# Optimization experiments

Measured on AMD Instinct MI355X. Metric: run time of the kernel, lower is better.

Reference implementation:

```python
import jax, jax.numpy as jnp
import numpy as np

T, B, OBS, LS, H, NA = 256, 1024, 128, 128, 128, 18


def setup_inputs() -> dict:
    key = jax.random.key(0)
    ks = jax.random.split(key, 20)
    rn = lambda i, shape, sc: jax.random.normal(ks[i], shape, dtype=jnp.float32) * sc
    return {
        "x": jax.random.normal(ks[0], (T * B, OBS), dtype=jnp.float32),
        "done": (jax.random.uniform(ks[1], (T * B,)) < 0.05).astype(jnp.float32),
        "h0": rn(2, (1, B, H), 0.1),
        "c0": rn(3, (1, B, H), 0.1),
        # MLP encoder: obs -> 128 -> 32 -> lstm_size
        "W1": rn(4, (128, OBS), 0.1), "b1": jnp.zeros((128,), jnp.float32),
        "W2": rn(5, (32, 128), 0.1), "b2": jnp.zeros((32,), jnp.float32),
        "W3": rn(6, (LS, 32), 0.1), "b3": jnp.zeros((LS,), jnp.float32),
        # LSTM params, PyTorch gate order [i, f, g, o]
        "Wih": rn(7, (4 * H, LS), 0.1), "Whh": rn(8, (4 * H, H), 0.1),
        "bih": jnp.zeros((4 * H,), jnp.float32), "bhh": jnp.zeros((4 * H,), jnp.float32),
        "Wa": rn(9, (NA, H), 0.01), "ba": jnp.zeros((NA,), jnp.float32),
        "Wc": rn(10, (1, H), 0.1), "bc": jnp.zeros((1,), jnp.float32),
    }


def reference(x, done, h0, c0, W1, b1, W2, b2, W3, b3, Wih, Whh, bih, bhh, Wa, ba, Wc, bc):
    # MLP encoder (self.network)
    hid = jax.nn.relu(x @ W1.T + b1)
    hid = jax.nn.relu(hid @ W2.T + b2)
    hid = jax.nn.relu(hid @ W3.T + b3)           # [T*B, LS]
    Bsz = h0.shape[1]
    hid = hid.reshape(-1, Bsz, hid.shape[-1])    # [T, B, LS]
    d = done.reshape(-1, Bsz)                    # [T, B]

    Hh = h0.shape[-1]

    def step(carry, inp):
        h, c = carry
        xt, dt = inp
        m = (1.0 - dt)[:, None]                  # reset mask
        h = h * m
        c = c * m
        gates = xt @ Wih.T + bih + h @ Whh.T + bhh   # [B, 4H]
        i = jax.nn.sigmoid(gates[:, :Hh])
        f = jax.nn.sigmoid(gates[:, Hh:2 * Hh])
        g = jnp.tanh(gates[:, 2 * Hh:3 * Hh])
        o = jax.nn.sigmoid(gates[:, 3 * Hh:])
        c = f * c + i * g
        h = o * jnp.tanh(c)
        return (h, c), h

    (hN, cN), hs = jax.lax.scan(step, (h0[0], c0[0]), (hid, d))
    flat = hs.reshape(-1, Hh)                    # [T*B, H]
    logits = flat @ Wa.T + ba                    # actor head
    value = flat @ Wc.T + bc                     # critic head
    return jnp.concatenate([logits, value], axis=-1)  # [T*B, NA+1]
```

## Files before the change

### kernel.cpp

```cpp
#include <hip/hip_runtime.h>
#include <hip/hip_bf16.h>

typedef unsigned short u16;
typedef unsigned int u32;
typedef __attribute__((ext_vector_type(8))) short short8;
typedef __attribute__((ext_vector_type(4))) float f4;
typedef __attribute__((ext_vector_type(4))) u32 u4;

#define MFMA(a, b, c) __builtin_amdgcn_mfma_f32_16x16x32_bf16((a), (b), (c), 0, 0, 0)

#define TT 256
#define BB 1024
#define NN (TT * BB)
#define NCHUNK (NN / 16)
#define WS_HID3 0
#define WS_WF   (NN * 128)
#define OFF_W1  0
#define OFF_W2  16384
#define OFF_W3  20480
#define OFF_WIH 24576
#define OFF_WHH 90112
#define OFF_WA  155648
#define WF_TOT  159744

static __device__ __forceinline__ u16 f2bf(float f) {
    u32 u = __float_as_uint(f);
    u32 r = (u + 0x7FFFu + ((u >> 16) & 1u)) >> 16;
    return (u16)r;
}
static __device__ __forceinline__ short8 pack8(f4 a, f4 b) {
    short8 r;
    r[0] = (short)f2bf(a[0]); r[1] = (short)f2bf(a[1]);
    r[2] = (short)f2bf(a[2]); r[3] = (short)f2bf(a[3]);
    r[4] = (short)f2bf(b[0]); r[5] = (short)f2bf(b[1]);
    r[6] = (short)f2bf(b[2]); r[7] = (short)f2bf(b[3]);
    return r;
}
static __device__ __forceinline__ short8 u4_to_s8(u4 v) {
    union { u4 u; short8 s; } t; t.u = v; return t.s;
}
static __device__ __forceinline__ float sigf(float x) {
    return __builtin_amdgcn_rcpf(1.f + __builtin_amdgcn_exp2f(-1.442695040888963f * x));
}
static __device__ __forceinline__ float tanhf_fast(float x) {
    return 2.f * __builtin_amdgcn_rcpf(1.f + __builtin_amdgcn_exp2f(-2.885390081777927f * x)) - 1.f;
}

static __device__ void convW128(const float* src, int Nn, u16* dst, int tid, int nth) {
    int tot = Nn * 128;
    for (int d = tid; d < tot; d += nth) {
        int j = d & 7, l = (d >> 3) & 63, ck = d >> 9;
        int kc = ck & 3, nt = ck >> 2;
        int n = nt * 16 + (l & 15), k = kc * 32 + ((l >> 4) << 3) + j;
        dst[d] = f2bf(src[n * 128 + k]);
    }
}
static __device__ void convW32(const float* src, int Nn, u16* dst, int tid, int nth) {
    int tot = Nn * 32;
    for (int d = tid; d < tot; d += nth) {
        int j = d & 7, l = (d >> 3) & 63, nt = d >> 9;
        int n = nt * 16 + (l & 15), k = ((l >> 4) << 3) + j;
        dst[d] = f2bf(src[n * 32 + k]);
    }
}

__global__ void k0_conv(const float* __restrict__ W1, const float* __restrict__ W2,
                        const float* __restrict__ W3, const float* __restrict__ Wih,
                        const float* __restrict__ Whh, const float* __restrict__ Wa,
                        const float* __restrict__ Wc, u16* __restrict__ wf) {
    int tid = blockIdx.x * blockDim.x + threadIdx.x;
    int nth = gridDim.x * blockDim.x;
    convW128(W1, 128, wf + OFF_W1, tid, nth);
    convW128(W2, 32, wf + OFF_W2, tid, nth);
    convW32(W3, 128, wf + OFF_W3, tid, nth);
    convW128(Wih, 512, wf + OFF_WIH, tid, nth);
    convW128(Whh, 512, wf + OFF_WHH, tid, nth);
    for (int d = tid; d < 32 * 128; d += nth) {
        int j = d & 7, l = (d >> 3) & 63, ck = d >> 9;
        int kc = ck & 3, nt = ck >> 2;
        int n = nt * 16 + (l & 15), k = kc * 32 + ((l >> 4) << 3) + j;
        float v = (n < 18) ? Wa[n * 128 + k] : ((n == 18) ? Wc[k] : 0.f);
        wf[OFF_WA + d] = f2bf(v);
    }
}

__global__ __launch_bounds__(256) void k1_enc(
    const float* __restrict__ x, const float* __restrict__ b1, const float* __restrict__ b2,
    const float* __restrict__ b3, const u16* __restrict__ wf, u16* __restrict__ hid3f) {
    __shared__ __align__(16) u16 scr[4][2560];

    int tid = threadIdx.x, wv = tid >> 6, lane = tid & 63;
    int m = lane & 15, q = lane >> 4;
    u16* s1 = scr[wv];
    u16* s2 = scr[wv] + 2048;
    const short8* W1v = (const short8*)(wf + OFF_W1);
    const short8* W2v = (const short8*)(wf + OFF_W2);
    const short8* W3v = (const short8*)(wf + OFF_W3);
    int wid = blockIdx.x * 4 + wv;

    for (int it = 0; it < 8; ++it) {
        int c = wid + it * 2048;
        short8 a1[4];
        const float* xr = x + (size_t)(c * 16 + m) * 128 + q * 8;
#pragma unroll
        for (int kc = 0; kc < 4; ++kc) {
            f4 f0 = *(const f4*)(xr + kc * 32);
            f4 f1 = *(const f4*)(xr + kc * 32 + 4);
            a1[kc] = pack8(f0, f1);
        }
#pragma unroll
        for (int nt = 0; nt < 8; ++nt) {
            f4 acc = {0.f, 0.f, 0.f, 0.f};
#pragma unroll
            for (int kc = 0; kc < 4; ++kc) acc = MFMA(a1[kc], W1v[(nt * 4 + kc) * 64 + lane], acc);
            int col = nt * 16 + m;
            float bb = b1[col];
            int base = (col >> 5) * 512 + ((col >> 3) & 3) * 128 + (col & 7);
#pragma unroll
            for (int p = 0; p < 4; ++p) {
                float v = acc[p] + bb; v = v > 0.f ? v : 0.f;
                s1[base + (q * 4 + p) * 8] = f2bf(v);
            }
        }
        __syncthreads();
        short8 a2[4];
#pragma unroll
        for (int kc = 0; kc < 4; ++kc) a2[kc] = *(const short8*)(s1 + kc * 512 + lane * 8);
#pragma unroll
        for (int nt = 0; nt < 2; ++nt) {
            f4 acc = {0.f, 0.f, 0.f, 0.f};
#pragma unroll
            for (int kc = 0; kc < 4; ++kc) acc = MFMA(a2[kc], W2v[(nt * 4 + kc) * 64 + lane], acc);
            int col = nt * 16 + m;
            float bb = b2[col];
            int base = (col >> 3) * 128 + (col & 7);
#pragma unroll
            for (int p = 0; p < 4; ++p) {
                float v = acc[p] + bb; v = v > 0.f ? v : 0.f;
                s2[base + (q * 4 + p) * 8] = f2bf(v);
            }
        }
        __syncthreads();
        short8 a3 = *(const short8*)(s2 + lane * 8);
#pragma unroll
        for (int nt = 0; nt < 8; ++nt) {
            f4 acc = {0.f, 0.f, 0.f, 0.f};
            acc = MFMA(a3, W3v[nt * 64 + lane], acc);
            int col = nt * 16 + m;
            float bb = b3[col];
            int base = (col >> 5) * 512 + ((col >> 3) & 3) * 128 + (col & 7);
#pragma unroll
            for (int p = 0; p < 4; ++p) {
                float v = acc[p] + bb; v = v > 0.f ? v : 0.f;
                s1[base + (q * 4 + p) * 8] = f2bf(v);
            }
        }
        __syncthreads();
        u4* dst = (u4*)hid3f + (size_t)c * 256;
#pragma unroll
        for (int kc = 0; kc < 4; ++kc) dst[kc * 64 + lane] = *(const u4*)(s1 + kc * 512 + lane * 8);
    }
}

__global__ __launch_bounds__(512) void k3_lstm(
    u16* __restrict__ hws,
    const u16* __restrict__ wf, const float* __restrict__ bih, const float* __restrict__ bhh,
    const float* __restrict__ done, const float* __restrict__ h0, const float* __restrict__ c0) {
    __shared__ __align__(16) u16 hbuf[2][2048];
    __shared__ __align__(16) float dls[4096];

    int tid = threadIdx.x, wv = tid >> 6, lane = tid & 63;
    int u15 = lane & 15, q = lane >> 4;
    int u = wv * 16 + u15;
    int rb = blockIdx.x * 16;
    const short8* WHv = (const short8*)(wf + OFF_WHH);
    const short8* WIv = (const short8*)(wf + OFF_WIH);

    short8 wh[4][4], wi[4][4];
#pragma unroll
    for (int g = 0; g < 4; ++g)
#pragma unroll
        for (int kc = 0; kc < 4; ++kc) {
            int nt = g * 8 + wv;
            wh[g][kc] = WHv[(nt * 4 + kc) * 64 + lane];
            wi[g][kc] = WIv[(nt * 4 + kc) * 64 + lane];
        }
    float bg[4];
#pragma unroll
    for (int g = 0; g < 4; ++g) bg[g] = bih[g * 128 + u] + bhh[g * 128 + u];

    for (int i = tid; i < 4096; i += 512) {
        int t = i >> 4, r = i & 15;
        dls[i] = 1.0f - done[(size_t)t * BB + rb + r];
    }
    float cst[4];
#pragma unroll
    for (int k = 0; k < 4; ++k) {
        int r = 4 * q + k;
        cst[k] = c0[(size_t)(rb + r) * 128 + u];
        float hv = h0[(size_t)(rb + r) * 128 + u];
        hbuf[0][(u >> 5) * 512 + (((u >> 3) & 3) * 16 + r) * 8 + (u & 7)] = f2bf(hv);
    }
    const u4* h3 = (const u4*)hws;
    u4 xf[4];
#pragma unroll
    for (int kc = 0; kc < 4; ++kc)
        xf[kc] = h3[((size_t)blockIdx.x * 4 + kc) * 64 + lane];
    __syncthreads();

    for (int t = 0; t < TT; ++t) {
        const u16* hc = hbuf[t & 1];
        u16* hn = hbuf[(t + 1) & 1];
        short8 ah[4];
#pragma unroll
        for (int kc = 0; kc < 4; ++kc) ah[kc] = *(const short8*)(hc + kc * 512 + lane * 8);
        f4 aH[4], aX[4];
#pragma unroll
        for (int g = 0; g < 4; ++g) { aH[g] = (f4){0.f, 0.f, 0.f, 0.f}; aX[g] = (f4){0.f, 0.f, 0.f, 0.f}; }
#pragma unroll
        for (int kc = 0; kc < 4; ++kc) {
            short8 xs = u4_to_s8(xf[kc]);
#pragma unroll
            for (int g = 0; g < 4; ++g) {
                aH[g] = MFMA(ah[kc], wh[g][kc], aH[g]);
                aX[g] = MFMA(xs, wi[g][kc], aX[g]);
            }
        }
        if (t < TT - 1) {
#pragma unroll
            for (int kc = 0; kc < 4; ++kc)
                xf[kc] = h3[(((size_t)(t + 1) * 64 + blockIdx.x) * 4 + kc) * 64 + lane];
        }
        f4 dm = *(const f4*)(dls + t * 16 + 4 * q);
#pragma unroll
        for (int k = 0; k < 4; ++k) {
            float mm = dm[k];
            float ip = aX[0][k] + bg[0] + mm * aH[0][k];
            float fp = aX[1][k] + bg[1] + mm * aH[1][k];
            float gp = aX[2][k] + bg[2] + mm * aH[2][k];
            float op = aX[3][k] + bg[3] + mm * aH[3][k];
            float ii = sigf(ip), ff = sigf(fp), gg = tanhf_fast(gp), oo = sigf(op);
            float cc = ff * (mm * cst[k]) + ii * gg;
            cst[k] = cc;
            float hh = oo * tanhf_fast(cc);
            hn[(u >> 5) * 512 + (((u >> 3) & 3) * 16 + (4 * q + k)) * 8 + (u & 7)] = f2bf(hh);
        }
        __syncthreads();
        if (wv < 4) {
            u4 v = *(const u4*)(hn + wv * 512 + lane * 8);
            ((u4*)hws)[(((size_t)t * 64 + blockIdx.x) * 4 + wv) * 64 + lane] = v;
        }
    }
}

__global__ __launch_bounds__(256) void k4_heads(
    const u16* __restrict__ hsf, const u16* __restrict__ wf,
    const float* __restrict__ ba, const float* __restrict__ bc, float* __restrict__ out) {
    int tid = threadIdx.x, wv = tid >> 6, lane = tid & 63;
    int m = lane & 15, q = lane >> 4;
    int wid = blockIdx.x * 4 + wv;
    const short8* WAv = (const short8*)(wf + OFF_WA);
    short8 wab[2][4];
#pragma unroll
    for (int nt = 0; nt < 2; ++nt)
#pragma unroll
        for (int kc = 0; kc < 4; ++kc) wab[nt][kc] = WAv[(nt * 4 + kc) * 64 + lane];
    const short8* A = (const short8*)hsf;
    for (int it = 0; it < 8; ++it) {
        int c = wid + it * 2048;
        short8 a[4];
#pragma unroll
        for (int kc = 0; kc < 4; ++kc) a[kc] = A[((size_t)c * 4 + kc) * 64 + lane];
#pragma unroll
        for (int nt = 0; nt < 2; ++nt) {
            f4 acc = {0.f, 0.f, 0.f, 0.f};
#pragma unroll
            for (int kc = 0; kc < 4; ++kc) acc = MFMA(a[kc], wab[nt][kc], acc);
            int col = nt * 16 + m;
            if (col < 19) {
                float bb = (col < 18) ? ba[col] : bc[0];
#pragma unroll
                for (int p = 0; p < 4; ++p)
                    out[(size_t)(c * 16 + q * 4 + p) * 19 + col] = acc[p] + bb;
            }
        }
    }
}

extern "C" void kernel_launch(void* const* d_in, const int* in_sizes, int n_in,
                              void* d_out, int out_size, void* d_ws, size_t ws_size,
                              hipStream_t stream) {
    const float* x    = (const float*)d_in[0];
    const float* done = (const float*)d_in[1];
    const float* h0   = (const float*)d_in[2];
    const float* c0   = (const float*)d_in[3];
    const float* W1   = (const float*)d_in[4];
    const float* b1   = (const float*)d_in[5];
    const float* W2   = (const float*)d_in[6];
    const float* b2   = (const float*)d_in[7];
    const float* W3   = (const float*)d_in[8];
    const float* b3   = (const float*)d_in[9];
    const float* Wih  = (const float*)d_in[10];
    const float* Whh  = (const float*)d_in[11];
    const float* bih  = (const float*)d_in[12];
    const float* bhh  = (const float*)d_in[13];
    const float* Wa   = (const float*)d_in[14];
    const float* ba   = (const float*)d_in[15];
    const float* Wc   = (const float*)d_in[16];
    const float* bc   = (const float*)d_in[17];
    float* out = (float*)d_out;

    u16* ws = (u16*)d_ws;
    u16* hid3f = ws + WS_HID3;
    u16* wf    = ws + WS_WF;

    hipLaunchKernelGGL(k0_conv, dim3(128), dim3(256), 0, stream,
                       W1, W2, W3, Wih, Whh, Wa, Wc, wf);
    hipLaunchKernelGGL(k1_enc, dim3(512), dim3(256), 0, stream,
                       x, b1, b2, b3, wf, hid3f);
    hipLaunchKernelGGL(k3_lstm, dim3(64), dim3(512), 0, stream,
                       hid3f, wf, bih, bhh, done, h0, c0);
    hipLaunchKernelGGL(k4_heads, dim3(512), dim3(256), 0, stream,
                       hid3f, wf, ba, bc, out);
}
```

Baseline: 577.6 us.

## Precompute LSTM input projections in a parallel GEMM before the recurrent scan

Adds a k2_xg kernel that computes x@Wih^T plus both biases for all timesteps in parallel and stores the result as bf16 gate pre-activations in workspace. The scan kernel then only performs the h@Whh MFMAs on its serial critical path, prefetching precomputed gates two steps ahead. The encoder is relaunched with one chunk per wave and no intra-block barriers, and the scan barrier becomes an LDS-only waitcnt plus s_barrier. The cost is a large extra workspace buffer with heavy global traffic, and the gate inputs are rounded to bf16. The new path is used only when the workspace is large enough, otherwise the old fused LSTM kernel runs.

```diff
diff --git a/kernel.cpp b/kernel.cpp
--- a/kernel.cpp
+++ b/kernel.cpp
@@ -6,13 +6,13 @@
 typedef __attribute__((ext_vector_type(8))) short short8;
 typedef __attribute__((ext_vector_type(4))) float f4;
 typedef __attribute__((ext_vector_type(4))) u32 u4;
+typedef __attribute__((ext_vector_type(2))) u32 u2;
 
 #define MFMA(a, b, c) __builtin_amdgcn_mfma_f32_16x16x32_bf16((a), (b), (c), 0, 0, 0)
 
 #define TT 256
 #define BB 1024
 #define NN (TT * BB)
-#define NCHUNK (NN / 16)
 #define WS_HID3 0
 #define WS_WF   (NN * 128)
 #define OFF_W1  0
@@ -22,6 +22,9 @@
 #define OFF_WHH 90112
 #define OFF_WA  155648
 #define WF_TOT  159744
+#define WS_XG   (WS_WF + WF_TOT)
+#define XG_U16  ((size_t)NN * 512)
+#define WS_NEED_BIG 335863808ULL
 
 static __device__ __forceinline__ u16 f2bf(float f) {
     u32 u = __float_as_uint(f);
@@ -44,6 +47,9 @@
 }
 static __device__ __forceinline__ float tanhf_fast(float x) {
     return 2.f * __builtin_amdgcn_rcpf(1.f + __builtin_amdgcn_exp2f(-2.885390081777927f * x)) - 1.f;
+}
+static __device__ __forceinline__ void lds_barrier() {
+    asm volatile("s_waitcnt lgkmcnt(0)\n\ts_barrier" ::: "memory");
 }
 
 static __device__ void convW128(const float* src, int Nn, u16* dst, int tid, int nth) {
@@ -96,76 +102,195 @@
     const short8* W1v = (const short8*)(wf + OFF_W1);
     const short8* W2v = (const short8*)(wf + OFF_W2);
     const short8* W3v = (const short8*)(wf + OFF_W3);
-    int wid = blockIdx.x * 4 + wv;
-
-    for (int it = 0; it < 8; ++it) {
-        int c = wid + it * 2048;
-        short8 a1[4];
-        const float* xr = x + (size_t)(c * 16 + m) * 128 + q * 8;
-#pragma unroll
-        for (int kc = 0; kc < 4; ++kc) {
-            f4 f0 = *(const f4*)(xr + kc * 32);
-            f4 f1 = *(const f4*)(xr + kc * 32 + 4);
-            a1[kc] = pack8(f0, f1);
-        }
-#pragma unroll
-        for (int nt = 0; nt < 8; ++nt) {
+    int c = blockIdx.x * 4 + wv;
+
+    short8 a1[4];
+    const float* xr = x + (size_t)(c * 16 + m) * 128 + q * 8;
+#pragma unroll
+    for (int kc = 0; kc < 4; ++kc) {
+        f4 f0 = *(const f4*)(xr + kc * 32);
+        f4 f1 = *(const f4*)(xr + kc * 32 + 4);
+        a1[kc] = pack8(f0, f1);
+    }
+#pragma unroll
+    for (int nt = 0; nt < 8; ++nt) {
+        f4 acc = {0.f, 0.f, 0.f, 0.f};
+#pragma unroll
+        for (int kc = 0; kc < 4; ++kc) acc = MFMA(a1[kc], W1v[(nt * 4 + kc) * 64 + lane], acc);
+        int col = nt * 16 + m;
+        float bb = b1[col];
+        int base = (col >> 5) * 512 + ((col >> 3) & 3) * 128 + (col & 7);
+#pragma unroll
+        for (int p = 0; p < 4; ++p) {
+            float v = acc[p] + bb; v = v > 0.f ? v : 0.f;
+            s1[base + (q * 4 + p) * 8] = f2bf(v);
+        }
+    }
+    short8 a2[4];
+#pragma unroll
+    for (int kc = 0; kc < 4; ++kc) a2[kc] = *(const short8*)(s1 + kc * 512 + lane * 8);
+#pragma unroll
+    for (int nt = 0; nt < 2; ++nt) {
+        f4 acc = {0.f, 0.f, 0.f, 0.f};
+#pragma unroll
+        for (int kc = 0; kc < 4; ++kc) acc = MFMA(a2[kc], W2v[(nt * 4 + kc) * 64 + lane], acc);
+        int col = nt * 16 + m;
+        float bb = b2[col];
+        int base = (col >> 3) * 128 + (col & 7);
+#pragma unroll
+        for (int p = 0; p < 4; ++p) {
+            float v = acc[p] + bb; v = v > 0.f ? v : 0.f;
+            s2[base + (q * 4 + p) * 8] = f2bf(v);
+        }
+    }
+    short8 a3 = *(const short8*)(s2 + lane * 8);
+#pragma unroll
+    for (int nt = 0; nt < 8; ++nt) {
+        f4 acc = {0.f, 0.f, 0.f, 0.f};
+        acc = MFMA(a3, W3v[nt * 64 + lane], acc);
+        int col = nt * 16 + m;
+        float bb = b3[col];
+        int base = (col >> 5) * 512 + ((col >> 3) & 3) * 128 + (col & 7);
+#pragma unroll
+        for (int p = 0; p < 4; ++p) {
+            float v = acc[p] + bb; v = v > 0.f ? v : 0.f;
+            s1[base + (q * 4 + p) * 8] = f2bf(v);
+        }
+    }
+    u4* dst = (u4*)hid3f + (size_t)c * 256;
+#pragma unroll
+    for (int kc = 0; kc < 4; ++kc) dst[kc * 64 + lane] = *(const u4*)(s1 + kc * 512 + lane * 8);
+}
+
+__global__ __launch_bounds__(512) void k2_xg(
+    const u16* __restrict__ hid3f, const u16* __restrict__ wf,
+    const float* __restrict__ bih, const float* __restrict__ bhh, u16* __restrict__ xg) {
+    int tid = threadIdx.x, wv = tid >> 6, lane = tid & 63;
+    int m = lane & 15;
+    const short8* WIv = (const short8*)(wf + OFF_WIH);
+    short8 wb[4][4];
+    float bias[4];
+#pragma unroll
+    for (int j = 0; j < 4; ++j) {
+        int nt = wv * 4 + j;
+#pragma unroll
+        for (int kc = 0; kc < 4; ++kc) wb[j][kc] = WIv[(nt * 4 + kc) * 64 + lane];
+        bias[j] = bih[nt * 16 + m] + bhh[nt * 16 + m];
+    }
+    const u4* A = (const u4*)hid3f;
+    for (int i = 0; i < 64; ++i) {
+        size_t c = (size_t)blockIdx.x * 64 + i;
+        u4 av[4];
+#pragma unroll
+        for (int kc = 0; kc < 4; ++kc) av[kc] = A[(c * 4 + kc) * 64 + lane];
+#pragma unroll
+        for (int j = 0; j < 4; ++j) {
             f4 acc = {0.f, 0.f, 0.f, 0.f};
 #pragma unroll
-            for (int kc = 0; kc < 4; ++kc) acc = MFMA(a1[kc], W1v[(nt * 4 + kc) * 64 + lane], acc);
-            int col = nt * 16 + m;
-            float bb = b1[col];
-            int base = (col >> 5) * 512 + ((col >> 3) & 3) * 128 + (col & 7);
-#pragma unroll
-            for (int p = 0; p < 4; ++p) {
-                float v = acc[p] + bb; v = v > 0.f ? v : 0.f;
-                s1[base + (q * 4 + p) * 8] = f2bf(v);
+            for (int kc = 0; kc < 4; ++kc) acc = MFMA(u4_to_s8(av[kc]), wb[j][kc], acc);
+            int nt = wv * 4 + j;
+            u2 pk;
+            float v0 = acc[0] + bias[j], v1 = acc[1] + bias[j];
+            float v2 = acc[2] + bias[j], v3 = acc[3] + bias[j];
+            pk[0] = ((u32)f2bf(v1) << 16) | (u32)f2bf(v0);
+            pk[1] = ((u32)f2bf(v3) << 16) | (u32)f2bf(v2);
+            *(u2*)(xg + ((c * 32 + (size_t)nt) * 64 + lane) * 4) = pk;
+        }
+    }
+}
+
+__global__ __launch_bounds__(512) void k3_scan(
+    const u16* __restrict__ xg, u16* __restrict__ hsout, const u16* __restrict__ wf,
+    const float* __restrict__ done, const float* __restrict__ h0, const float* __restrict__ c0) {
+    __shared__ __align__(16) u16 hbuf[2][2048];
+    __shared__ __align__(16) float dls[4096];
+
+    int tid = threadIdx.x, wv = tid >> 6, lane = tid & 63;
+    int m = lane & 15, q = lane >> 4;
+    int u = wv * 16 + m;
+    int rb = blockIdx.x * 16;
+    const short8* WHv = (const short8*)(wf + OFF_WHH);
+
+    short8 wh[4][4];
+#pragma unroll
+    for (int g = 0; g < 4; ++g)
+#pragma unroll
+        for (int kc = 0; kc < 4; ++kc)
+            wh[g][kc] = WHv[(((g * 8 + wv) * 4) + kc) * 64 + lane];
+
+    for (int i = tid; i < 4096; i += 512) {
+        int t = i >> 4, r = i & 15;
+        dls[i] = 1.0f - done[(size_t)t * BB + rb + r];
+    }
+    float cst[4];
+#pragma unroll
+    for (int k = 0; k < 4; ++k) {
+        int r = 4 * q + k;
+        cst[k] = c0[(size_t)(rb + r) * 128 + u];
+        float hv = h0[(size_t)(rb + r) * 128 + u];
+        hbuf[0][(u >> 5) * 512 + (((u >> 3) & 3) * 16 + r) * 8 + (u & 7)] = f2bf(hv);
+    }
+    const u2* XG = (const u2*)xg;
+    u2 xbuf[2][4];
+#pragma unroll
+    for (int g = 0; g < 4; ++g) {
+        xbuf[0][g] = XG[((size_t)(0 * 64 + blockIdx.x) * 32 + g * 8 + wv) * 64 + lane];
+        xbuf[1][g] = XG[((size_t)(1 * 64 + blockIdx.x) * 32 + g * 8 + wv) * 64 + lane];
+    }
+    __syncthreads();
+
+    for (int t = 0; t < TT; ++t) {
+        const u16* hc = hbuf[t & 1];
+        u16* hn = hbuf[(t + 1) & 1];
+        short8 ah[4];
+#pragma unroll
+        for (int kc = 0; kc < 4; ++kc) ah[kc] = *(const short8*)(hc + kc * 512 + lane * 8);
+        f4 aH[4];
+#pragma unroll
+        for (int g = 0; g < 4; ++g) aH[g] = (f4){0.f, 0.f, 0.f, 0.f};
+#pragma unroll
+        for (int kc = 0; kc < 4; ++kc)
+#pragma unroll
+            for (int g = 0; g < 4; ++g) aH[g] = MFMA(ah[kc], wh[g][kc], aH[g]);
+
+        u2 xcur[4];
+#pragma unroll
+        for (int g = 0; g < 4; ++g) xcur[g] = xbuf[t & 1][g];
+        int tp = (t + 2 < TT) ? (t + 2) : (TT - 1);
+#pragma unroll
+        for (int g = 0; g < 4; ++g)
+            xbuf[t & 1][g] = XG[((size_t)(tp * 64 + blockIdx.x) * 32 + g * 8 + wv) * 64 + lane];
+
+        f4 dm = *(const f4*)(dls + t * 16 + 4 * q);
+#pragma unroll
+        for (int k = 0; k < 4; ++k) {
+            float mm = dm[k];
+            float pre[4];
+#pragma unroll
+            for (int g = 0; g < 4; ++g) {
+                u32 w = (k < 2) ? xcur[g][0] : xcur[g][1];
+                u32 bits = (k & 1) ? (w & 0xFFFF0000u) : (w << 16);
+                pre[g] = __uint_as_float(bits) + mm * aH[g][k];
             }
-        }
-        __syncthreads();
-        short8 a2[4];
-#pragma unroll
-        for (int kc = 0; kc < 4; ++kc) a2[kc] = *(const short8*)(s1 + kc * 512 + lane * 8);
-#pragma unroll
-        for (int nt = 0; nt < 2; ++nt) {
-            f4 acc = {0.f, 0.f, 0.f, 0.f};
-#pragma unroll
-            for (int kc = 0; kc < 4; ++kc) acc = MFMA(a2[kc], W2v[(nt * 4 + kc) * 64 + lane], acc);
-            int col = nt * 16 + m;
-            float bb = b2[col];
-            int base = (col >> 3) * 128 + (col & 7);
-#pragma unroll
-            for (int p = 0; p < 4; ++p) {
-                float v = acc[p] + bb; v = v > 0.f ? v : 0.f;
-                s2[base + (q * 4 + p) * 8] = f2bf(v);
-            }
-        }
-        __syncthreads();
-        short8 a3 = *(const short8*)(s2 + lane * 8);
-#pragma unroll
-        for (int nt = 0; nt < 8; ++nt) {
-            f4 acc = {0.f, 0.f, 0.f, 0.f};
-            acc = MFMA(a3, W3v[nt * 64 + lane], acc);
-            int col = nt * 16 + m;
-            float bb = b3[col];
-            int base = (col >> 5) * 512 + ((col >> 3) & 3) * 128 + (col & 7);
-#pragma unroll
-            for (int p = 0; p < 4; ++p) {
-                float v = acc[p] + bb; v = v > 0.f ? v : 0.f;
-                s1[base + (q * 4 + p) * 8] = f2bf(v);
-            }
-        }
-        __syncthreads();
-        u4* dst = (u4*)hid3f + (size_t)c * 256;
-#pragma unroll
-        for (int kc = 0; kc < 4; ++kc) dst[kc * 64 + lane] = *(const u4*)(s1 + kc * 512 + lane * 8);
+            float ii = sigf(pre[0]), ff = sigf(pre[1]);
+            float gg = tanhf_fast(pre[2]), oo = sigf(pre[3]);
+            float cc = ff * (mm * cst[k]) + ii * gg;
+            cst[k] = cc;
+            float hh = oo * tanhf_fast(cc);
+            hn[(u >> 5) * 512 + (((u >> 3) & 3) * 16 + (4 * q + k)) * 8 + (u & 7)] = f2bf(hh);
+        }
+        lds_barrier();
+        if (wv < 4) {
+            u4 v = *(const u4*)(hn + wv * 512 + lane * 8);
+            ((u4*)hsout)[(((size_t)t * 64 + blockIdx.x) * 4 + wv) * 64 + lane] = v;
+        }
     }
 }
 
 __global__ __launch_bounds__(512) void k3_lstm(
-    u16* __restrict__ hws,
-    const u16* __restrict__ wf, const float* __restrict__ bih, const float* __restrict__ bhh,
-    const float* __restrict__ done, const float* __restrict__ h0, const float* __restrict__ c0) {
+    u16* __restrict__ hws, const u16* __restrict__ wf, const float* __restrict__ bih,
+    const float* __restrict__ bhh, const float* __restrict__ done,
+    const float* __restrict__ h0, const float* __restrict__ c0) {
     __shared__ __align__(16) u16 hbuf[2][2048];
     __shared__ __align__(16) float dls[4096];
 
@@ -204,8 +329,7 @@
     const u4* h3 = (const u4*)hws;
     u4 xf[4];
 #pragma unroll
-    for (int kc = 0; kc < 4; ++kc)
-        xf[kc] = h3[((size_t)blockIdx.x * 4 + kc) * 64 + lane];
+    for (int kc = 0; kc < 4; ++kc) xf[kc] = h3[((size_t)blockIdx.x * 4 + kc) * 64 + lane];
     __syncthreads();
 
     for (int t = 0; t < TT; ++t) {
@@ -245,7 +369,7 @@
             float hh = oo * tanhf_fast(cc);
             hn[(u >> 5) * 512 + (((u >> 3) & 3) * 16 + (4 * q + k)) * 8 + (u & 7)] = f2bf(hh);
         }
-        __syncthreads();
+        lds_barrier();
         if (wv < 4) {
             u4 v = *(const u4*)(hn + wv * 512 + lane * 8);
             ((u4*)hws)[(((size_t)t * 64 + blockIdx.x) * 4 + wv) * 64 + lane] = v;
@@ -313,13 +437,21 @@
     u16* ws = (u16*)d_ws;
     u16* hid3f = ws + WS_HID3;
     u16* wf    = ws + WS_WF;
+    u16* xg    = ws + WS_XG;
 
     hipLaunchKernelGGL(k0_conv, dim3(128), dim3(256), 0, stream,
                        W1, W2, W3, Wih, Whh, Wa, Wc, wf);
-    hipLaunchKernelGGL(k1_enc, dim3(512), dim3(256), 0, stream,
+    hipLaunchKernelGGL(k1_enc, dim3(4096), dim3(256), 0, stream,
                        x, b1, b2, b3, wf, hid3f);
-    hipLaunchKernelGGL(k3_lstm, dim3(64), dim3(512), 0, stream,
-                       hid3f, wf, bih, bhh, done, h0, c0);
+    if (ws_size >= WS_NEED_BIG) {
+        hipLaunchKernelGGL(k2_xg, dim3(256), dim3(512), 0, stream,
+                           hid3f, wf, bih, bhh, xg);
+        hipLaunchKernelGGL(k3_scan, dim3(64), dim3(512), 0, stream,
+                           xg, hid3f, wf, done, h0, c0);
+    } else {
+        hipLaunchKernelGGL(k3_lstm, dim3(64), dim3(512), 0, stream,
+                           hid3f, wf, bih, bhh, done, h0, c0);
+    }
     hipLaunchKernelGGL(k4_heads, dim3(512), dim3(256), 0, stream,
                        hid3f, wf, ba, bc, out);
 }
```

After: 717.2 us. 24.2% more time.

## Hoist LSTM input projection into encoder and spread scan over more blocks

Applied to the files above, without the earlier changes.

The input-to-gate projection (Wih·x + biases) moves out of the sequential LSTM loop into the parallel encoder kernel, which writes packed bf16 gate pre-activations to a large workspace. The scan then spreads over 256 blocks of 4 batch rows each, doing only the Whh MFMA per step and exchanging partial results through LDS. Gate weights and biases are pre-scaled by log2(e) factors to save multiplies in the activations, and syncthreads is replaced by a custom LDS barrier. This costs extra workspace traffic (about 256 MB of gate data) and a fallback path is kept for when the workspace is too small.

```diff
diff --git a/kernel.cpp b/kernel.cpp
--- a/kernel.cpp
+++ b/kernel.cpp
@@ -6,15 +6,16 @@
 typedef __attribute__((ext_vector_type(8))) short short8;
 typedef __attribute__((ext_vector_type(4))) float f4;
 typedef __attribute__((ext_vector_type(4))) u32 u4;
+typedef __attribute__((ext_vector_type(2))) u32 u2;
 
 #define MFMA(a, b, c) __builtin_amdgcn_mfma_f32_16x16x32_bf16((a), (b), (c), 0, 0, 0)
 
 #define TT 256
 #define BB 1024
 #define NN (TT * BB)
-#define NCHUNK (NN / 16)
-#define WS_HID3 0
-#define WS_WF   (NN * 128)
+#define SC1 1.4426950408889634f
+#define SC2 2.8853900817779268f
+
 #define OFF_W1  0
 #define OFF_W2  16384
 #define OFF_W3  20480
@@ -23,6 +24,10 @@
 #define OFF_WA  155648
 #define WF_TOT  159744
 
+#define WS_HS_OFF 134217728
+#define WS_WF_OFF 167772160
+#define WS_NEED_BIG 335863808ULL
+
 static __device__ __forceinline__ u16 f2bf(float f) {
     u32 u = __float_as_uint(f);
     u32 r = (u + 0x7FFFu + ((u >> 16) & 1u)) >> 16;
@@ -39,11 +44,17 @@
 static __device__ __forceinline__ short8 u4_to_s8(u4 v) {
     union { u4 u; short8 s; } t; t.u = v; return t.s;
 }
-static __device__ __forceinline__ float sigf(float x) {
-    return __builtin_amdgcn_rcpf(1.f + __builtin_amdgcn_exp2f(-1.442695040888963f * x));
-}
-static __device__ __forceinline__ float tanhf_fast(float x) {
-    return 2.f * __builtin_amdgcn_rcpf(1.f + __builtin_amdgcn_exp2f(-2.885390081777927f * x)) - 1.f;
+static __device__ __forceinline__ float sig2(float x) {
+    return __builtin_amdgcn_rcpf(1.f + __builtin_amdgcn_exp2f(-x));
+}
+static __device__ __forceinline__ float tanh2pre(float x) {
+    return 2.f * __builtin_amdgcn_rcpf(1.f + __builtin_amdgcn_exp2f(-x)) - 1.f;
+}
+static __device__ __forceinline__ float tanh_c(float x) {
+    return 2.f * __builtin_amdgcn_rcpf(1.f + __builtin_amdgcn_exp2f(-SC2 * x)) - 1.f;
+}
+static __device__ __forceinline__ void lds_barrier() {
+    asm volatile("s_waitcnt lgkmcnt(0)\n\ts_barrier" ::: "memory");
 }
 
 static __device__ void convW128(const float* src, int Nn, u16* dst, int tid, int nth) {
@@ -53,6 +64,16 @@
         int kc = ck & 3, nt = ck >> 2;
         int n = nt * 16 + (l & 15), k = kc * 32 + ((l >> 4) << 3) + j;
         dst[d] = f2bf(src[n * 128 + k]);
+    }
+}
+static __device__ void convW128s(const float* src, u16* dst, int tid, int nth) {
+    int tot = 512 * 128;
+    for (int d = tid; d < tot; d += nth) {
+        int j = d & 7, l = (d >> 3) & 63, ck = d >> 9;
+        int kc = ck & 3, nt = ck >> 2;
+        int n = nt * 16 + (l & 15), k = kc * 32 + ((l >> 4) << 3) + j;
+        float s = ((n >> 7) == 2) ? SC2 : SC1;
+        dst[d] = f2bf(src[n * 128 + k] * s);
     }
 }
 static __device__ void convW32(const float* src, int Nn, u16* dst, int tid, int nth) {
@@ -73,8 +94,8 @@
     convW128(W1, 128, wf + OFF_W1, tid, nth);
     convW128(W2, 32, wf + OFF_W2, tid, nth);
     convW32(W3, 128, wf + OFF_W3, tid, nth);
-    convW128(Wih, 512, wf + OFF_WIH, tid, nth);
-    convW128(Whh, 512, wf + OFF_WHH, tid, nth);
+    convW128s(Wih, wf + OFF_WIH, tid, nth);
+    convW128s(Whh, wf + OFF_WHH, tid, nth);
     for (int d = tid; d < 32 * 128; d += nth) {
         int j = d & 7, l = (d >> 3) & 63, ck = d >> 9;
         int kc = ck & 3, nt = ck >> 2;
@@ -84,10 +105,12 @@
     }
 }
 
-__global__ __launch_bounds__(256) void k1_enc(
+__global__ __launch_bounds__(256) void k1_fused(
     const float* __restrict__ x, const float* __restrict__ b1, const float* __restrict__ b2,
-    const float* __restrict__ b3, const u16* __restrict__ wf, u16* __restrict__ hid3f) {
+    const float* __restrict__ b3, const float* __restrict__ bih, const float* __restrict__ bhh,
+    const u16* __restrict__ wf, u2* __restrict__ xg) {
     __shared__ __align__(16) u16 scr[4][2560];
+    __shared__ float biasL[512];
 
     int tid = threadIdx.x, wv = tid >> 6, lane = tid & 63;
     int m = lane & 15, q = lane >> 4;
@@ -96,86 +119,297 @@
     const short8* W1v = (const short8*)(wf + OFF_W1);
     const short8* W2v = (const short8*)(wf + OFF_W2);
     const short8* W3v = (const short8*)(wf + OFF_W3);
+    const short8* WIv = (const short8*)(wf + OFF_WIH);
+    int c = blockIdx.x * 4 + wv;
+
+    for (int i = tid; i < 512; i += 256)
+        biasL[i] = (bih[i] + bhh[i]) * (((i >> 7) == 2) ? SC2 : SC1);
+
+    short8 a1[4];
+    const float* xr = x + (size_t)(c * 16 + m) * 128 + q * 8;
+#pragma unroll
+    for (int kc = 0; kc < 4; ++kc) {
+        f4 f0 = *(const f4*)(xr + kc * 32);
+        f4 f1 = *(const f4*)(xr + kc * 32 + 4);
+        a1[kc] = pack8(f0, f1);
+    }
+#pragma unroll
+    for (int nt = 0; nt < 8; ++nt) {
+        f4 acc = {0.f, 0.f, 0.f, 0.f};
+#pragma unroll
+        for (int kc = 0; kc < 4; ++kc) acc = MFMA(a1[kc], W1v[(nt * 4 + kc) * 64 + lane], acc);
+        int col = nt * 16 + m;
+        float bb = b1[col];
+        int base = (col >> 5) * 512 + ((col >> 3) & 3) * 128 + (col & 7);
+#pragma unroll
+        for (int p = 0; p < 4; ++p) {
+            float v = acc[p] + bb; v = v > 0.f ? v : 0.f;
+            s1[base + (q * 4 + p) * 8] = f2bf(v);
+        }
+    }
+    short8 a2[4];
+#pragma unroll
+    for (int kc = 0; kc < 4; ++kc) a2[kc] = *(const short8*)(s1 + kc * 512 + lane * 8);
+#pragma unroll
+    for (int nt = 0; nt < 2; ++nt) {
+        f4 acc = {0.f, 0.f, 0.f, 0.f};
+#pragma unroll
+        for (int kc = 0; kc < 4; ++kc) acc = MFMA(a2[kc], W2v[(nt * 4 + kc) * 64 + lane], acc);
+        int col = nt * 16 + m;
+        float bb = b2[col];
+        int base = (col >> 3) * 128 + (col & 7);
+#pragma unroll
+        for (int p = 0; p < 4; ++p) {
+            float v = acc[p] + bb; v = v > 0.f ? v : 0.f;
+            s2[base + (q * 4 + p) * 8] = f2bf(v);
+        }
+    }
+    short8 a3 = *(const short8*)(s2 + lane * 8);
+#pragma unroll
+    for (int nt = 0; nt < 8; ++nt) {
+        f4 acc = {0.f, 0.f, 0.f, 0.f};
+        acc = MFMA(a3, W3v[nt * 64 + lane], acc);
+        int col = nt * 16 + m;
+        float bb = b3[col];
+        int base = (col >> 5) * 512 + ((col >> 3) & 3) * 128 + (col & 7);
+#pragma unroll
+        for (int p = 0; p < 4; ++p) {
+            float v = acc[p] + bb; v = v > 0.f ? v : 0.f;
+            s1[base + (q * 4 + p) * 8] = f2bf(v);
+        }
+    }
+    __syncthreads();
+
+    short8 bfr[4];
+#pragma unroll
+    for (int kc = 0; kc < 4; ++kc) bfr[kc] = *(const short8*)(s1 + kc * 512 + lane * 8);
+    size_t R = (size_t)c * 16 + m;
+#pragma unroll
+    for (int uw = 0; uw < 8; ++uw) {
+        f4 acc[4];
+#pragma unroll
+        for (int g = 0; g < 4; ++g) acc[g] = (f4){0.f, 0.f, 0.f, 0.f};
+#pragma unroll
+        for (int kc = 0; kc < 4; ++kc) {
+#pragma unroll
+            for (int g = 0; g < 4; ++g) {
+                int nt = g * 8 + uw;
+                acc[g] = MFMA(WIv[(nt * 4 + kc) * 64 + lane], bfr[kc], acc[g]);
+            }
+        }
+        u4 st0, st1;
+#pragma unroll
+        for (int p = 0; p < 4; ++p) {
+            int u = uw * 16 + 4 * q + p;
+            u32 lo = ((u32)f2bf(acc[1][p] + biasL[128 + u]) << 16) |
+                     (u32)f2bf(acc[0][p] + biasL[u]);
+            u32 hi = ((u32)f2bf(acc[3][p] + biasL[384 + u]) << 16) |
+                     (u32)f2bf(acc[2][p] + biasL[256 + u]);
+            if (p < 2) { st0[2 * p] = lo; st0[2 * p + 1] = hi; }
+            else       { st1[2 * (p - 2)] = lo; st1[2 * (p - 2) + 1] = hi; }
+        }
+        u4* dst = (u4*)(xg + R * 128 + uw * 16 + 4 * q);
+        dst[0] = st0;
+        dst[1] = st1;
+    }
+}
+
+__global__ __launch_bounds__(512) void k3_scan(
+    const u2* __restrict__ xg, u16* __restrict__ hs, const u16* __restrict__ wf,
+    const float* __restrict__ done, const float* __restrict__ h0, const float* __restrict__ c0) {
+    __shared__ __align__(16) u16 hbuf[2][16 * 136];
+    __shared__ __align__(16) float pre[4 * 516];
+    __shared__ float dls[1024];
+
+    int tid = threadIdx.x, wv = tid >> 6, lane = tid & 63;
+    int m = lane & 15, q = lane >> 4;
+    int rb = blockIdx.x * 4;
+    const short8* WHv = (const short8*)(wf + OFF_WHH);
+
+    short8 wh[4][4];
+#pragma unroll
+    for (int g = 0; g < 4; ++g)
+#pragma unroll
+        for (int kc = 0; kc < 4; ++kc)
+            wh[g][kc] = WHv[(((g * 8 + wv) * 4) + kc) * 64 + lane];
+
+    for (int i = tid; i < 2 * 12 * 136; i += 512) {
+        int b = i / 1632, rem = i % 1632;
+        hbuf[b][(4 + rem / 136) * 136 + (rem % 136)] = 0;
+    }
+    for (int i = tid; i < 1024; i += 512)
+        dls[i] = 1.0f - done[(size_t)(i >> 2) * BB + rb + (i & 3)];
+
+    int r = tid >> 7, u = tid & 127;
+    float cst = c0[(size_t)(rb + r) * 128 + u];
+    hbuf[0][r * 136 + u] = f2bf(h0[(size_t)(rb + r) * 128 + u]);
+
+    u2 xp0 = xg[(size_t)blockIdx.x * 512 + tid];
+    u2 xp1 = xg[(size_t)131072 + (size_t)blockIdx.x * 512 + tid];
+    __syncthreads();
+
+    for (int t = 0; t < TT; ++t) {
+        const u16* hc = hbuf[t & 1];
+        u16* hn = hbuf[(t + 1) & 1];
+        short8 bh[4];
+#pragma unroll
+        for (int kc = 0; kc < 4; ++kc)
+            bh[kc] = *(const short8*)(hc + m * 136 + kc * 32 + q * 8);
+        f4 aH[4];
+#pragma unroll
+        for (int g = 0; g < 4; ++g) aH[g] = (f4){0.f, 0.f, 0.f, 0.f};
+#pragma unroll
+        for (int kc = 0; kc < 4; ++kc)
+#pragma unroll
+            for (int g = 0; g < 4; ++g) aH[g] = MFMA(wh[g][kc], bh[kc], aH[g]);
+
+        int tp = (t + 2 < TT) ? (t + 2) : (TT - 1);
+        u2 xnew = xg[(size_t)tp * 131072 + (size_t)blockIdx.x * 512 + tid];
+
+        if (m < 4) {
+#pragma unroll
+            for (int g = 0; g < 4; ++g)
+#pragma unroll
+                for (int p = 0; p < 4; ++p)
+                    pre[m * 516 + (wv * 16 + 4 * q + p) * 4 + g] = aH[g][p];
+        }
+        lds_barrier();
+
+        f4 pv = *(const f4*)(pre + r * 516 + u * 4);
+        float mm = dls[t * 4 + r];
+        u32 w0 = xp0[0], w1 = xp0[1];
+        float ip = __uint_as_float(w0 << 16)          + mm * pv[0];
+        float fp = __uint_as_float(w0 & 0xFFFF0000u)  + mm * pv[1];
+        float gp = __uint_as_float(w1 << 16)          + mm * pv[2];
+        float op = __uint_as_float(w1 & 0xFFFF0000u)  + mm * pv[3];
+        float ii = sig2(ip), ff = sig2(fp), gg = tanh2pre(gp), oo = sig2(op);
+        float cc = ff * (mm * cst) + ii * gg;
+        cst = cc;
+        float hh = oo * tanh_c(cc);
+        u16 hb = f2bf(hh);
+        hn[r * 136 + u] = hb;
+        hs[((size_t)t * BB + rb + r) * 128 + u] = hb;
+        xp0 = xp1; xp1 = xnew;
+        lds_barrier();
+    }
+}
+
+__global__ __launch_bounds__(256) void k4_heads_plain(
+    const u16* __restrict__ hs, const u16* __restrict__ wf,
+    const float* __restrict__ ba, const float* __restrict__ bc, float* __restrict__ out) {
+    int tid = threadIdx.x, wv = tid >> 6, lane = tid & 63;
+    int m = lane & 15, q = lane >> 4;
     int wid = blockIdx.x * 4 + wv;
-
+    const short8* WAv = (const short8*)(wf + OFF_WA);
+    short8 wab[2][4];
+#pragma unroll
+    for (int nt = 0; nt < 2; ++nt)
+#pragma unroll
+        for (int kc = 0; kc < 4; ++kc) wab[nt][kc] = WAv[(nt * 4 + kc) * 64 + lane];
     for (int it = 0; it < 8; ++it) {
         int c = wid + it * 2048;
-        short8 a1[4];
-        const float* xr = x + (size_t)(c * 16 + m) * 128 + q * 8;
-#pragma unroll
-        for (int kc = 0; kc < 4; ++kc) {
-            f4 f0 = *(const f4*)(xr + kc * 32);
-            f4 f1 = *(const f4*)(xr + kc * 32 + 4);
-            a1[kc] = pack8(f0, f1);
-        }
-#pragma unroll
-        for (int nt = 0; nt < 8; ++nt) {
-            f4 acc = {0.f, 0.f, 0.f, 0.f};
-#pragma unroll
-            for (int kc = 0; kc < 4; ++kc) acc = MFMA(a1[kc], W1v[(nt * 4 + kc) * 64 + lane], acc);
-            int col = nt * 16 + m;
-            float bb = b1[col];
-            int base = (col >> 5) * 512 + ((col >> 3) & 3) * 128 + (col & 7);
-#pragma unroll
-            for (int p = 0; p < 4; ++p) {
-                float v = acc[p] + bb; v = v > 0.f ? v : 0.f;
-                s1[base + (q * 4 + p) * 8] = f2bf(v);
-            }
-        }
-        __syncthreads();
-        short8 a2[4];
-#pragma unroll
-        for (int kc = 0; kc < 4; ++kc) a2[kc] = *(const short8*)(s1 + kc * 512 + lane * 8);
+        const u16* row = hs + ((size_t)c * 16 + m) * 128 + q * 8;
+        short8 a[4];
+#pragma unroll
+        for (int kc = 0; kc < 4; ++kc) a[kc] = *(const short8*)(row + kc * 32);
 #pragma unroll
         for (int nt = 0; nt < 2; ++nt) {
             f4 acc = {0.f, 0.f, 0.f, 0.f};
 #pragma unroll
-            for (int kc = 0; kc < 4; ++kc) acc = MFMA(a2[kc], W2v[(nt * 4 + kc) * 64 + lane], acc);
+            for (int kc = 0; kc < 4; ++kc) acc = MFMA(a[kc], wab[nt][kc], acc);
             int col = nt * 16 + m;
-            float bb = b2[col];
-            int base = (col >> 3) * 128 + (col & 7);
-#pragma unroll
-            for (int p = 0; p < 4; ++p) {
-                float v = acc[p] + bb; v = v > 0.f ? v : 0.f;
-                s2[base + (q * 4 + p) * 8] = f2bf(v);
+            if (col < 19) {
+                float bb = (col < 18) ? ba[col] : bc[0];
+#pragma unroll
+                for (int p = 0; p < 4; ++p)
+                    out[(size_t)(c * 16 + q * 4 + p) * 19 + col] = acc[p] + bb;
             }
         }
-        __syncthreads();
-        short8 a3 = *(const short8*)(s2 + lane * 8);
-#pragma unroll
-        for (int nt = 0; nt < 8; ++nt) {
-            f4 acc = {0.f, 0.f, 0.f, 0.f};
-            acc = MFMA(a3, W3v[nt * 64 + lane], acc);
-            int col = nt * 16 + m;
-            float bb = b3[col];
-            int base = (col >> 5) * 512 + ((col >> 3) & 3) * 128 + (col & 7);
-#pragma unroll
-            for (int p = 0; p < 4; ++p) {
-                float v = acc[p] + bb; v = v > 0.f ? v : 0.f;
-                s1[base + (q * 4 + p) * 8] = f2bf(v);
-            }
-        }
-        __syncthreads();
-        u4* dst = (u4*)hid3f + (size_t)c * 256;
-#pragma unroll
-        for (int kc = 0; kc < 4; ++kc) dst[kc * 64 + lane] = *(const u4*)(s1 + kc * 512 + lane * 8);
-    }
+    }
+}
+
+__global__ __launch_bounds__(256) void k1_enc(
+    const float* __restrict__ x, const float* __restrict__ b1, const float* __restrict__ b2,
+    const float* __restrict__ b3, const u16* __restrict__ wf, u16* __restrict__ hid3f) {
+    __shared__ __align__(16) u16 scr[4][2560];
+    int tid = threadIdx.x, wv = tid >> 6, lane = tid & 63;
+    int m = lane & 15, q = lane >> 4;
+    u16* s1 = scr[wv];
+    u16* s2 = scr[wv] + 2048;
+    const short8* W1v = (const short8*)(wf + OFF_W1);
+    const short8* W2v = (const short8*)(wf + OFF_W2);
+    const short8* W3v = (const short8*)(wf + OFF_W3);
+    int c = blockIdx.x * 4 + wv;
+    short8 a1[4];
+    const float* xr = x + (size_t)(c * 16 + m) * 128 + q * 8;
+#pragma unroll
+    for (int kc = 0; kc < 4; ++kc) {
+        f4 f0 = *(const f4*)(xr + kc * 32);
+        f4 f1 = *(const f4*)(xr + kc * 32 + 4);
+        a1[kc] = pack8(f0, f1);
+    }
+#pragma unroll
+    for (int nt = 0; nt < 8; ++nt) {
+        f4 acc = {0.f, 0.f, 0.f, 0.f};
+#pragma unroll
+        for (int kc = 0; kc < 4; ++kc) acc = MFMA(a1[kc], W1v[(nt * 4 + kc) * 64 + lane], acc);
+        int col = nt * 16 + m;
+        float bb = b1[col];
+        int base = (col >> 5) * 512 + ((col >> 3) & 3) * 128 + (col & 7);
+#pragma unroll
+        for (int p = 0; p < 4; ++p) {
+            float v = acc[p] + bb; v = v > 0.f ? v : 0.f;
+            s1[base + (q * 4 + p) * 8] = f2bf(v);
+        }
+    }
+    short8 a2[4];
+#pragma unroll
+    for (int kc = 0; kc < 4; ++kc) a2[kc] = *(const short8*)(s1 + kc * 512 + lane * 8);
+#pragma unroll
+    for (int nt = 0; nt < 2; ++nt) {
+        f4 acc = {0.f, 0.f, 0.f, 0.f};
+#pragma unroll
+        for (int kc = 0; kc < 4; ++kc) acc = MFMA(a2[kc], W2v[(nt * 4 + kc) * 64 + lane], acc);
+        int col = nt * 16 + m;
+        float bb = b2[col];
+        int base = (col >> 3) * 128 + (col & 7);
+#pragma unroll
+        for (int p = 0; p < 4; ++p) {
+            float v = acc[p] + bb; v = v > 0.f ? v : 0.f;
+            s2[base + (q * 4 + p) * 8] = f2bf(v);
+        }
+    }
+    short8 a3 = *(const short8*)(s2 + lane * 8);
+#pragma unroll
+    for (int nt = 0; nt < 8; ++nt) {
+        f4 acc = {0.f, 0.f, 0.f, 0.f};
+        acc = MFMA(a3, W3v[nt * 64 + lane], acc);
+        int col = nt * 16 + m;
+        float bb = b3[col];
+        int base = (col >> 5) * 512 + ((col >> 3) & 3) * 128 + (col & 7);
+#pragma unroll
+        for (int p = 0; p < 4; ++p) {
+            float v = acc[p] + bb; v = v > 0.f ? v : 0.f;
+            s1[base + (q * 4 + p) * 8] = f2bf(v);
+        }
+    }
+    u4* dst = (u4*)hid3f + (size_t)c * 256;
+#pragma unroll
+    for (int kc = 0; kc < 4; ++kc) dst[kc * 64 + lane] = *(const u4*)(s1 + kc * 512 + lane * 8);
 }
 
 __global__ __launch_bounds__(512) void k3_lstm(
-    u16* __restrict__ hws,
-    const u16* __restrict__ wf, const float* __restrict__ bih, const float* __restrict__ bhh,
-    const float* __restrict__ done, const float* __restrict__ h0, const float* __restrict__ c0) {
+    u16* __restrict__ hws, const u16* __restrict__ wf, const float* __restrict__ bih,
+    const float* __restrict__ bhh, const float* __restrict__ done,
+    const float* __restrict__ h0, const float* __restrict__ c0) {
     __shared__ __align__(16) u16 hbuf[2][2048];
     __shared__ __align__(16) float dls[4096];
-
     int tid = threadIdx.x, wv = tid >> 6, lane = tid & 63;
     int u15 = lane & 15, q = lane >> 4;
     int u = wv * 16 + u15;
     int rb = blockIdx.x * 16;
     const short8* WHv = (const short8*)(wf + OFF_WHH);
     const short8* WIv = (const short8*)(wf + OFF_WIH);
-
     short8 wh[4][4], wi[4][4];
 #pragma unroll
     for (int g = 0; g < 4; ++g)
@@ -187,8 +421,8 @@
         }
     float bg[4];
 #pragma unroll
-    for (int g = 0; g < 4; ++g) bg[g] = bih[g * 128 + u] + bhh[g * 128 + u];
-
+    for (int g = 0; g < 4; ++g)
+        bg[g] = (bih[g * 128 + u] + bhh[g * 128 + u]) * ((g == 2) ? SC2 : SC1);
     for (int i = tid; i < 4096; i += 512) {
         int t = i >> 4, r = i & 15;
         dls[i] = 1.0f - done[(size_t)t * BB + rb + r];
@@ -204,10 +438,8 @@
     const u4* h3 = (const u4*)hws;
     u4 xf[4];
 #pragma unroll
-    for (int kc = 0; kc < 4; ++kc)
-        xf[kc] = h3[((size_t)blockIdx.x * 4 + kc) * 64 + lane];
+    for (int kc = 0; kc < 4; ++kc) xf[kc] = h3[((size_t)blockIdx.x * 4 + kc) * 64 + lane];
     __syncthreads();
-
     for (int t = 0; t < TT; ++t) {
         const u16* hc = hbuf[t & 1];
         u16* hn = hbuf[(t + 1) & 1];
@@ -239,13 +471,13 @@
             float fp = aX[1][k] + bg[1] + mm * aH[1][k];
             float gp = aX[2][k] + bg[2] + mm * aH[2][k];
             float op = aX[3][k] + bg[3] + mm * aH[3][k];
-            float ii = sigf(ip), ff = sigf(fp), gg = tanhf_fast(gp), oo = sigf(op);
+            float ii = sig2(ip), ff = sig2(fp), gg = tanh2pre(gp), oo = sig2(op);
             float cc = ff * (mm * cst[k]) + ii * gg;
             cst[k] = cc;
-            float hh = oo * tanhf_fast(cc);
+            float hh = oo * tanh_c(cc);
             hn[(u >> 5) * 512 + (((u >> 3) & 3) * 16 + (4 * q + k)) * 8 + (u & 7)] = f2bf(hh);
         }
-        __syncthreads();
+        lds_barrier();
         if (wv < 4) {
             u4 v = *(const u4*)(hn + wv * 512 + lane * 8);
             ((u4*)hws)[(((size_t)t * 64 + blockIdx.x) * 4 + wv) * 64 + lane] = v;
@@ -253,7 +485,7 @@
     }
 }
 
-__global__ __launch_bounds__(256) void k4_heads(
+__global__ __launch_bounds__(256) void k4_heads_frag(
     const u16* __restrict__ hsf, const u16* __restrict__ wf,
     const float* __restrict__ ba, const float* __restrict__ bc, float* __restrict__ out) {
     int tid = threadIdx.x, wv = tid >> 6, lane = tid & 63;
@@ -309,17 +541,30 @@
     const float* Wc   = (const float*)d_in[16];
     const float* bc   = (const float*)d_in[17];
     float* out = (float*)d_out;
-
     u16* ws = (u16*)d_ws;
-    u16* hid3f = ws + WS_HID3;
-    u16* wf    = ws + WS_WF;
-
-    hipLaunchKernelGGL(k0_conv, dim3(128), dim3(256), 0, stream,
-                       W1, W2, W3, Wih, Whh, Wa, Wc, wf);
-    hipLaunchKernelGGL(k1_enc, dim3(512), dim3(256), 0, stream,
-                       x, b1, b2, b3, wf, hid3f);
-    hipLaunchKernelGGL(k3_lstm, dim3(64), dim3(512), 0, stream,
-                       hid3f, wf, bih, bhh, done, h0, c0);
-    hipLaunchKernelGGL(k4_heads, dim3(512), dim3(256), 0, stream,
-                       hid3f, wf, ba, bc, out);
-}
+
+    if (ws_size >= WS_NEED_BIG) {
+        u2*  xg = (u2*)ws;
+        u16* hs = ws + WS_HS_OFF;
+        u16* wf = ws + WS_WF_OFF;
+        hipLaunchKernelGGL(k0_conv, dim3(128), dim3(256), 0, stream,
+                           W1, W2, W3, Wih, Whh, Wa, Wc, wf);
+        hipLaunchKernelGGL(k1_fused, dim3(4096), dim3(256), 0, stream,
+                           x, b1, b2, b3, bih, bhh, wf, xg);
+        hipLaunchKernelGGL(k3_scan, dim3(256), dim3(512), 0, stream,
+                           xg, hs, wf, done, h0, c0);
+        hipLaunchKernelGGL(k4_heads_plain, dim3(512), dim3(256), 0, stream,
+                           hs, wf, ba, bc, out);
+    } else {
+        u16* hid3f = ws;
+        u16* wf    = ws + (size_t)NN * 128;
+        hipLaunchKernelGGL(k0_conv, dim3(128), dim3(256), 0, stream,
+                           W1, W2, W3, Wih, Whh, Wa, Wc, wf);
+        hipLaunchKernelGGL(k1_enc, dim3(4096), dim3(256), 0, stream,
+                           x, b1, b2, b3, wf, hid3f);
+        hipLaunchKernelGGL(k3_lstm, dim3(64), dim3(512), 0, stream,
+                           hid3f, wf, bih, bhh, done, h0, c0);
+        hipLaunchKernelGGL(k4_heads_frag, dim3(512), dim3(256), 0, stream,
+                           hid3f, wf, ba, bc, out);
+    }
+}
```

After: 598.8 us. +3.7%, slower.
